# Optimization experiments

Hardware: AMD Instinct MI355X
Metric: run time of the kernel (lower is better)

Reference implementation:

```python
import jax, jax.numpy as jnp
import numpy as np

B, N, D, G = 128, 36, 512, 2  # batch, num_bboxs, wrd_embed_size, num_glimpses
NEG = -1e10


def setup_inputs() -> dict:
    key = jax.random.key(0)
    k1, k2, k3 = jax.random.split(key, 3)
    obj_repr = jax.random.normal(k1, (B, N, D), dtype=jnp.float32)
    # attn_glimpse[0]: nn.Linear(num_bboxs * wrd_embed_size, num_glimpses)
    W = jax.random.normal(k2, (G, N * D), dtype=jnp.float32) * 0.02
    b = jnp.zeros((G,), dtype=jnp.float32)
    bboxs_mask = jax.random.randint(k3, (B, N), 0, 2).astype(bool)
    bboxs_mask = bboxs_mask.at[:, 0].set(True)  # at least one valid box per row
    return {"obj_repr": obj_repr, "W": W, "b": b, "bboxs_mask": bboxs_mask}


def reference(obj_repr, W, b, bboxs_mask):
    """Faithful port of QGenModel.self_diff_attention."""
    Bv, Nv, Dv = obj_repr.shape
    # pairwise object differences, gated by the query object: [B, N, N, D]
    diff = obj_repr[:, :, None, :] * (obj_repr[:, :, None, :] - obj_repr[:, None, :, :])
    flat = diff.reshape(Bv, Nv, Nv * Dv)              # [B, N, N*D]
    logits = flat @ W.T + b                            # [B, N, G]
    logits = jnp.where(bboxs_mask[:, :, None], logits, NEG)
    weight = jax.nn.softmax(logits, axis=1)            # softmax over box axis (dim=1)
    # weight.transpose(1,2) @ obj_repr  ->  [B, G, D]
    vis_repr = jnp.einsum('bng,bnd->bgd', weight, obj_repr)
    return vis_repr.reshape(Bv, -1)                    # [B, G*D]
```

## Files before the change

kernel.cpp:

```cpp
#include <hip/hip_runtime.h>
#include <hip/hip_bf16.h>


#define QB 128
#define QN 36
#define QD 512
#define QG 2

__global__ __launch_bounds__(QD) void qgen_self_diff_attn(
    const float* __restrict__ obj,
    const float* __restrict__ W,
    const float* __restrict__ bias,
    const int* __restrict__ mask,
    float* __restrict__ out)
{
    __shared__ float s_T[QG][QD];
    __shared__ float s_S[QG][QD];
    __shared__ float s_logit[QG][QN];
    __shared__ float s_w[QG][QN];

    const int b = blockIdx.x;
    const int t = threadIdx.x;
    const int wave = t >> 6;
    const int lane = t & 63;

    const float* ob = obj + (size_t)b * QN * QD;

    float o[QN];
    float T0 = 0.f, T1 = 0.f, S0 = 0.f, S1 = 0.f;
    #pragma unroll
    for (int m = 0; m < QN; ++m) {
        o[m] = ob[m * QD + t];
        float w0 = W[0 * QN * QD + m * QD + t];
        float w1 = W[1 * QN * QD + m * QD + t];
        T0 = fmaf(w0, o[m], T0);  T1 = fmaf(w1, o[m], T1);
        S0 += w0;                 S1 += w1;
    }
    s_T[0][t] = T0;  s_T[1][t] = T1;
    s_S[0][t] = S0;  s_S[1][t] = S1;
    __syncthreads();

    for (int n = wave; n < QN; n += 8) {
        float a0 = 0.f, a1 = 0.f;
        #pragma unroll
        for (int k = 0; k < QD / 64; ++k) {
            int d = lane + k * 64;
            float ov = ob[n * QD + d];
            float oo = ov * ov;
            a0 += oo * s_S[0][d] - ov * s_T[0][d];
            a1 += oo * s_S[1][d] - ov * s_T[1][d];
        }
        #pragma unroll
        for (int off = 32; off; off >>= 1) {
            a0 += __shfl_down(a0, off);
            a1 += __shfl_down(a1, off);
        }
        if (lane == 0) {
            bool mk = mask[b * QN + n] != 0;
            s_logit[0][n] = mk ? a0 + bias[0] : -1e10f;
            s_logit[1][n] = mk ? a1 + bias[1] : -1e10f;
        }
    }
    __syncthreads();

    if (wave < QG) {
        float v = (lane < QN) ? s_logit[wave][lane] : -1e30f;
        float mx = v;
        #pragma unroll
        for (int off = 32; off; off >>= 1)
            mx = fmaxf(mx, __shfl_xor(mx, off));
        float e = (lane < QN) ? __expf(v - mx) : 0.f;
        float sum = e;
        #pragma unroll
        for (int off = 32; off; off >>= 1)
            sum += __shfl_xor(sum, off);
        if (lane < QN) s_w[wave][lane] = e / sum;
    }
    __syncthreads();

    float v0 = 0.f, v1 = 0.f;
    #pragma unroll
    for (int n = 0; n < QN; ++n) {
        v0 = fmaf(s_w[0][n], o[n], v0);
        v1 = fmaf(s_w[1][n], o[n], v1);
    }
    out[(size_t)b * QG * QD + 0 * QD + t] = v0;
    out[(size_t)b * QG * QD + 1 * QD + t] = v1;
}

extern "C" void kernel_launch(void* const* d_in, const int* in_sizes, int n_in,
                              void* d_out, int out_size, void* d_ws, size_t ws_size,
                              hipStream_t stream) {
    const float* obj  = (const float*)d_in[0];
    const float* W    = (const float*)d_in[1];
    const float* bias = (const float*)d_in[2];
    const int*   mask = (const int*)d_in[3];
    float* out = (float*)d_out;

    qgen_self_diff_attn<<<QB, QD, 0, stream>>>(obj, W, bias, mask, out);
}
```

Before: 68.75 us.

## Split glimpses across blocks to double grid size

Launches one block per (batch, glimpse) pair instead of one per batch, so each block computes a single glimpse's logits, softmax and weighted sum. This doubles the block count from 128 to 256 to fill more of the device's compute units and lowers per-thread register and shared-memory use. In exchange, obj_repr is read twice (once per glimpse block) and the per-batch work is duplicated for loading and the diff reduction.

```diff
diff --git a/kernel.cpp b/kernel.cpp
--- a/kernel.cpp
+++ b/kernel.cpp
@@ -14,57 +14,54 @@
     const int* __restrict__ mask,
     float* __restrict__ out)
 {
-    __shared__ float s_T[QG][QD];
-    __shared__ float s_S[QG][QD];
-    __shared__ float s_logit[QG][QN];
-    __shared__ float s_w[QG][QN];
+    __shared__ float s_T[QD];
+    __shared__ float s_S[QD];
+    __shared__ float s_logit[QN];
+    __shared__ float s_w[QN];
 
-    const int b = blockIdx.x;
+    const int bid = blockIdx.x;
+    const int b = bid & (QB - 1);
+    const int g = bid >> 7;
     const int t = threadIdx.x;
     const int wave = t >> 6;
     const int lane = t & 63;
 
     const float* ob = obj + (size_t)b * QN * QD;
+    const float* wg = W + (size_t)g * QN * QD;
 
     float o[QN];
-    float T0 = 0.f, T1 = 0.f, S0 = 0.f, S1 = 0.f;
+    float T = 0.f, S = 0.f;
     #pragma unroll
     for (int m = 0; m < QN; ++m) {
         o[m] = ob[m * QD + t];
-        float w0 = W[0 * QN * QD + m * QD + t];
-        float w1 = W[1 * QN * QD + m * QD + t];
-        T0 = fmaf(w0, o[m], T0);  T1 = fmaf(w1, o[m], T1);
-        S0 += w0;                 S1 += w1;
+        float w = wg[m * QD + t];
+        T = fmaf(w, o[m], T);
+        S += w;
     }
-    s_T[0][t] = T0;  s_T[1][t] = T1;
-    s_S[0][t] = S0;  s_S[1][t] = S1;
+    s_T[t] = T;
+    s_S[t] = S;
     __syncthreads();
 
     for (int n = wave; n < QN; n += 8) {
-        float a0 = 0.f, a1 = 0.f;
+        float a = 0.f;
         #pragma unroll
         for (int k = 0; k < QD / 64; ++k) {
             int d = lane + k * 64;
             float ov = ob[n * QD + d];
-            float oo = ov * ov;
-            a0 += oo * s_S[0][d] - ov * s_T[0][d];
-            a1 += oo * s_S[1][d] - ov * s_T[1][d];
+            a += ov * ov * s_S[d] - ov * s_T[d];
         }
         #pragma unroll
-        for (int off = 32; off; off >>= 1) {
-            a0 += __shfl_down(a0, off);
-            a1 += __shfl_down(a1, off);
-        }
+        for (int off = 32; off; off >>= 1)
+            a += __shfl_down(a, off);
         if (lane == 0) {
             bool mk = mask[b * QN + n] != 0;
-            s_logit[0][n] = mk ? a0 + bias[0] : -1e10f;
-            s_logit[1][n] = mk ? a1 + bias[1] : -1e10f;
+            s_logit[n] = mk ? a + bias[g] : -1e10f;
         }
     }
     __syncthreads();
 
-    if (wave < QG) {
-        float v = (lane < QN) ? s_logit[wave][lane] : -1e30f;
+    if (wave == 0) {
+        float v = (lane < QN) ? s_logit[lane] : -1e30f;
         float mx = v;
         #pragma unroll
         for (int off = 32; off; off >>= 1)
@@ -74,18 +71,15 @@
         #pragma unroll
         for (int off = 32; off; off >>= 1)
             sum += __shfl_xor(sum, off);
-        if (lane < QN) s_w[wave][lane] = e / sum;
+        if (lane < QN) s_w[lane] = e / sum;
     }
     __syncthreads();
 
-    float v0 = 0.f, v1 = 0.f;
+    float v = 0.f;
     #pragma unroll
-    for (int n = 0; n < QN; ++n) {
-        v0 = fmaf(s_w[0][n], o[n], v0);
-        v1 = fmaf(s_w[1][n], o[n], v1);
-    }
-    out[(size_t)b * QG * QD + 0 * QD + t] = v0;
-    out[(size_t)b * QG * QD + 1 * QD + t] = v1;
+    for (int n = 0; n < QN; ++n)
+        v = fmaf(s_w[n], o[n], v);
+    out[(size_t)b * QG * QD + (size_t)g * QD + t] = v;
 }
 
 extern "C" void kernel_launch(void* const* d_in, const int* in_sizes, int n_in,
@@ -97,5 +91,5 @@
     const int*   mask = (const int*)d_in[3];
     float* out = (float*)d_out;
 
-    qgen_self_diff_attn<<<QB, QD, 0, stream>>>(obj, W, bias, mask, out);
+    qgen_self_diff_attn<<<QB * QG, QD, 0, stream>>>(obj, W, bias, mask, out);
 }
```

Result: no change. 67.57 us (-1.7%).
